# Performance work log

Hardware: AMD Instinct MI355X
Metric: run time of the kernel (lower is better)

## Reference

```python
import jax, jax.numpy as jnp
import numpy as np


def setup_inputs() -> dict:
    key = jax.random.key(0)
    k1, k2 = jax.random.split(key)
    B, C, H = 1024, 1000, 512  # batch, classes, hidden
    y = jax.random.normal(k1, (B, C), dtype=jnp.float32)
    w = jax.random.normal(k2, (C, H), dtype=jnp.float32)
    epsilon = jnp.ones((), dtype=jnp.float32)
    lipschitz = jnp.ones((), dtype=jnp.float32)
    return {"y": y, "w": w, "epsilon": epsilon, "lipschitz": lipschitz}


def reference(y, w, epsilon, lipschitz):
    # y: [B, C] logits; w: [C, H] final-layer weight
    kW = lipschitz * w.T                      # [H, C]
    j = jnp.argmax(y, axis=1)                 # [B]
    y_j = jnp.max(y, axis=1, keepdims=True)   # [B, 1]
    kW_j = kW.T[j]                            # [B, H] gather of argmax column
    kW_ij = kW_j[:, :, None] - kW[None]       # [B, H, C] broadcast difference
    sq = jnp.sum(kW_ij * kW_ij, axis=1)       # [B, C]
    # safe sqrt (value identical; avoids NaN grad at the exact-zero j column)
    K_ij = jnp.where(sq > 0, jnp.sqrt(jnp.where(sq > 0, sq, 1.0)), 0.0)
    y_bot_i = y + epsilon * K_ij              # [B, C]
    y_bot_i = jnp.where(y == y_j, -jnp.inf, y_bot_i)
    y_bot = jnp.max(y_bot_i, axis=1, keepdims=True)  # [B, 1]
    return jnp.concatenate([y, y_bot], axis=1)       # [B, C+1]
```

## Files before the change

### kernel.cpp

```cpp
#include <hip/hip_runtime.h>
#include <math.h>

#define B_SZ 1024
#define C_SZ 1000
#define H_SZ 512


typedef __attribute__((ext_vector_type(8))) short bf16x8;
typedef __attribute__((ext_vector_type(4))) float f32x4;

__global__ __launch_bounds__(256) void k_prep(
    const float* __restrict__ y, const float* __restrict__ w,
    int* __restrict__ jv, float* __restrict__ ymax,
    float* __restrict__ wnorm, short* __restrict__ wbf,
    float* __restrict__ out) {
    const int r = blockIdx.x;
    const int tid = threadIdx.x;
    if (r < 250) {
        const int wave = tid >> 6, lane = tid & 63;
        const int c = r * 4 + wave;
        const float* row = w + c * H_SZ;
        float4 a = *(const float4*)(row + lane * 8);
        float4 b = *(const float4*)(row + lane * 8 + 4);
        float f[8] = {a.x, a.y, a.z, a.w, b.x, b.y, b.z, b.w};
        unsigned short u[8];
        float s = 0.f;
#pragma unroll
        for (int i = 0; i < 8; ++i) {
            s += f[i] * f[i];
            unsigned v = __float_as_uint(f[i]);
            v += 0x7fffu + ((v >> 16) & 1u);
            u[i] = (unsigned short)(v >> 16);
        }
        uint4 pk;
        pk.x = (unsigned)u[0] | ((unsigned)u[1] << 16);
        pk.y = (unsigned)u[2] | ((unsigned)u[3] << 16);
        pk.z = (unsigned)u[4] | ((unsigned)u[5] << 16);
        pk.w = (unsigned)u[6] | ((unsigned)u[7] << 16);
        *(uint4*)(wbf + c * H_SZ + lane * 8) = pk;
#pragma unroll
        for (int off = 32; off; off >>= 1) s += __shfl_down(s, off, 64);
        if (lane == 0) wnorm[c] = s;
    } else {
        const int b = r - 250;
        const float* yrow = y + b * C_SZ;
        float* orow = out + b * (C_SZ + 1);
        float best = -INFINITY;
        int bidx = 0x7fffffff;
        if (tid < 250) {
            float4 v = *(const float4*)(yrow + tid * 4);
            float e[4] = {v.x, v.y, v.z, v.w};
#pragma unroll
            for (int i = 0; i < 4; ++i) {
                orow[tid * 4 + i] = e[i];
                if (e[i] > best) { best = e[i]; bidx = tid * 4 + i; }
            }
        }
        const int lane = tid & 63;
#pragma unroll
        for (int off = 32; off; off >>= 1) {
            float ov = __shfl_down(best, off, 64);
            int oi = __shfl_down(bidx, off, 64);
            if (ov > best || (ov == best && oi < bidx)) { best = ov; bidx = oi; }
        }
        __shared__ float sv[4];
        __shared__ int si[4];
        if (lane == 0) { sv[tid >> 6] = best; si[tid >> 6] = bidx; }
        __syncthreads();
        if (tid == 0) {
            float bv = sv[0]; int bi = si[0];
#pragma unroll
            for (int k = 1; k < 4; ++k) {
                if (sv[k] > bv || (sv[k] == bv && si[k] < bi)) { bv = sv[k]; bi = si[k]; }
            }
            jv[b] = bi;
            ymax[b] = bv;
        }
    }
}

#define KC 128
#define RS 136
__global__ __launch_bounds__(256) void k_main(
    const float* __restrict__ y, const short* __restrict__ wbf,
    const float* __restrict__ eps_p, const float* __restrict__ lip_p,
    const int* __restrict__ jv, const float* __restrict__ ymax,
    const float* __restrict__ wnorm, float* __restrict__ part) {
    __shared__ __align__(16) short Bs[64 * RS];
    __shared__ float snj[64];
    __shared__ float sym[64];

    const int t = threadIdx.x;
    const int bx = blockIdx.x, by = blockIdx.y;
    const int b0 = by * 64, c0 = bx * 64;

    if (t < 64) {
        int j = jv[b0 + t];
        snj[t] = wnorm[j];
        sym[t] = ymax[b0 + t];
    }

    const int wv = t >> 6, lane = t & 63;
    const int col = lane & 15, quad = lane >> 4;

    const int ja = jv[b0 + wv * 16 + col];
    const short* ag = wbf + ja * H_SZ + quad * 8;
    bf16x8 areg[16];
#pragma unroll
    for (int k16 = 0; k16 < 16; ++k16)
        areg[k16] = *(const bf16x8*)(ag + k16 * 32);

    const int srow = t >> 2;
    const int sseg = t & 3;
    int crow = c0 + srow; if (crow > C_SZ - 1) crow = C_SZ - 1;
    const short* bgsrc = wbf + crow * H_SZ;

    uint4 pb[4];
#pragma unroll
    for (int p = 0; p < 4; ++p)
        pb[p] = *(const uint4*)(bgsrc + (sseg + p * 4) * 8);

    const short* brd = &Bs[col * RS + quad * 8];

    f32x4 acc[4] = {{0.f, 0.f, 0.f, 0.f},
                    {0.f, 0.f, 0.f, 0.f},
                    {0.f, 0.f, 0.f, 0.f},
                    {0.f, 0.f, 0.f, 0.f}};

#pragma unroll
    for (int ch = 0; ch < 4; ++ch) {
#pragma unroll
        for (int p = 0; p < 4; ++p)
            *(uint4*)&Bs[srow * RS + (sseg + p * 4) * 8] = pb[p];
        __syncthreads();
        if (ch < 3) {
            const int gbase = (ch + 1) * KC;
#pragma unroll
            for (int p = 0; p < 4; ++p)
                pb[p] = *(const uint4*)(bgsrc + gbase + (sseg + p * 4) * 8);
        }
#pragma unroll
        for (int ks = 0; ks < 4; ++ks) {
            bf16x8 af = areg[ch * 4 + ks];
#pragma unroll
            for (int ct = 0; ct < 4; ++ct) {
                bf16x8 bf = *(const bf16x8*)(brd + ct * 16 * RS + ks * 32);
                acc[ct] =
                    __builtin_amdgcn_mfma_f32_16x16x32_bf16(af, bf, acc[ct], 0, 0, 0);
            }
        }
        __syncthreads();
    }

    const float eps = *eps_p;
    const float L = *lip_p;
    const float L2 = L * L;
    float rmax[4];
#pragma unroll
    for (int i = 0; i < 4; ++i) {
        const int br = wv * 16 + quad * 4 + i;
        const int b = b0 + br;
        const float nj = snj[br];
        const float ym = sym[br];
        float m = -INFINITY;
#pragma unroll
        for (int ct = 0; ct < 4; ++ct) {
            const int cc = c0 + ct * 16 + col;
            if (cc < C_SZ) {
                const float yv = y[b * C_SZ + cc];
                const float nc = wnorm[cc];
                const float sq = L2 * (nj + nc - 2.0f * acc[ct][i]);
                const float K = sq > 0.f ? sqrtf(sq) : 0.f;
                const float cand = (yv == ym) ? -INFINITY : yv + eps * K;
                m = fmaxf(m, cand);
            }
        }
        rmax[i] = m;
    }
#pragma unroll
    for (int off = 8; off; off >>= 1)
#pragma unroll
        for (int i = 0; i < 4; ++i)
            rmax[i] = fmaxf(rmax[i], __shfl_xor(rmax[i], off, 64));
    if (col == 0) {
        float* slice = part + bx * B_SZ;
#pragma unroll
        for (int i = 0; i < 4; ++i)
            slice[b0 + wv * 16 + quad * 4 + i] = rmax[i];
    }
}

__global__ void k_final(const float* __restrict__ part,
                        float* __restrict__ out) {
    int b = blockIdx.x * 256 + threadIdx.x;
    if (b >= B_SZ) return;
    float m = -INFINITY;
#pragma unroll
    for (int s = 0; s < 16; ++s) m = fmaxf(m, part[s * B_SZ + b]);
    out[b * (C_SZ + 1) + C_SZ] = m;
}

extern "C" void kernel_launch(void* const* d_in, const int* in_sizes, int n_in,
                              void* d_out, int out_size, void* d_ws,
                              size_t ws_size, hipStream_t stream) {
    const float* y = (const float*)d_in[0];
    const float* w = (const float*)d_in[1];
    const float* eps = (const float*)d_in[2];
    const float* lip = (const float*)d_in[3];
    float* out = (float*)d_out;

    char* ws = (char*)d_ws;
    int* jv = (int*)ws;
    float* ymax = (float*)(ws + 4096);
    float* wnorm = (float*)(ws + 8192);
    float* part = (float*)(ws + 16384);
    short* wbf = (short*)(ws + 524288);

    k_prep<<<250 + B_SZ, 256, 0, stream>>>(y, w, jv, ymax, wnorm, wbf, out);
    k_main<<<dim3(16, 16), 256, 0, stream>>>(y, wbf, eps, lip, jv, ymax, wnorm,
                                             part);
    k_final<<<(B_SZ + 255) / 256, 256, 0, stream>>>(part, out);
}
```

Before: 79.28 us.

## Fuse prep, main and final kernels into one cooperative kernel with grid syncs

Merges the three kernels into a single cooperative launch of 256 blocks, using grid.sync() between the prep phase (bf16 conversion, norms, per-row argmax), the MFMA distance phase and the final row-max reduction. Row argmax now uses one wave per row instead of one block per row, so 256 blocks cover all 1024 rows. The aim is to remove two kernel launch gaps and the shared-memory cross-wave reduction. In exchange it adds grid-wide barrier costs, and the prep phase now runs on fewer blocks with more serial work per wave.

```diff
diff --git a/kernel.cpp b/kernel.cpp
--- a/kernel.cpp
+++ b/kernel.cpp
@@ -1,5 +1,8 @@
 #include <hip/hip_runtime.h>
+#include <hip/hip_cooperative_groups.h>
 #include <math.h>
+
+namespace cg = cooperative_groups;
 
 #define B_SZ 1024
 #define C_SZ 1000
@@ -9,16 +12,27 @@
 typedef __attribute__((ext_vector_type(8))) short bf16x8;
 typedef __attribute__((ext_vector_type(4))) float f32x4;
 
-__global__ __launch_bounds__(256) void k_prep(
+#define KC 128
+#define RS 136
+
+__global__ __launch_bounds__(256) void k_fused(
     const float* __restrict__ y, const float* __restrict__ w,
+    const float* __restrict__ eps_p, const float* __restrict__ lip_p,
     int* __restrict__ jv, float* __restrict__ ymax,
     float* __restrict__ wnorm, short* __restrict__ wbf,
-    float* __restrict__ out) {
-    const int r = blockIdx.x;
-    const int tid = threadIdx.x;
-    if (r < 250) {
-        const int wave = tid >> 6, lane = tid & 63;
-        const int c = r * 4 + wave;
+    float* __restrict__ part, float* __restrict__ out) {
+    cg::grid_group grid = cg::this_grid();
+
+    __shared__ __align__(16) short Bs[64 * RS];
+    __shared__ float snj[64];
+    __shared__ float sym[64];
+
+    const int blk = blockIdx.x;
+    const int t = threadIdx.x;
+    const int wv = t >> 6, lane = t & 63;
+
+    if (blk < 250) {
+        const int c = blk * 4 + wv;
         const float* row = w + c * H_SZ;
         float4 a = *(const float4*)(row + lane * 8);
         float4 b = *(const float4*)(row + lane * 8 + 4);
@@ -41,57 +55,40 @@
 #pragma unroll
         for (int off = 32; off; off >>= 1) s += __shfl_down(s, off, 64);
         if (lane == 0) wnorm[c] = s;
-    } else {
-        const int b = r - 250;
+    }
+
+    {
+        const int b = blk * 4 + wv;
         const float* yrow = y + b * C_SZ;
         float* orow = out + b * (C_SZ + 1);
         float best = -INFINITY;
         int bidx = 0x7fffffff;
-        if (tid < 250) {
-            float4 v = *(const float4*)(yrow + tid * 4);
-            float e[4] = {v.x, v.y, v.z, v.w};
-#pragma unroll
-            for (int i = 0; i < 4; ++i) {
-                orow[tid * 4 + i] = e[i];
-                if (e[i] > best) { best = e[i]; bidx = tid * 4 + i; }
+#pragma unroll
+        for (int p = 0; p < 4; ++p) {
+            const int idx = lane + p * 64;
+            if (idx < 250) {
+                float4 v = *(const float4*)(yrow + idx * 4);
+                float e[4] = {v.x, v.y, v.z, v.w};
+#pragma unroll
+                for (int i = 0; i < 4; ++i) {
+                    orow[idx * 4 + i] = e[i];
+                    if (e[i] > best) { best = e[i]; bidx = idx * 4 + i; }
+                }
             }
         }
-        const int lane = tid & 63;
 #pragma unroll
         for (int off = 32; off; off >>= 1) {
             float ov = __shfl_down(best, off, 64);
             int oi = __shfl_down(bidx, off, 64);
             if (ov > best || (ov == best && oi < bidx)) { best = ov; bidx = oi; }
         }
-        __shared__ float sv[4];
-        __shared__ int si[4];
-        if (lane == 0) { sv[tid >> 6] = best; si[tid >> 6] = bidx; }
-        __syncthreads();
-        if (tid == 0) {
-            float bv = sv[0]; int bi = si[0];
-#pragma unroll
-            for (int k = 1; k < 4; ++k) {
-                if (sv[k] > bv || (sv[k] == bv && si[k] < bi)) { bv = sv[k]; bi = si[k]; }
-            }
-            jv[b] = bi;
-            ymax[b] = bv;
-        }
-    }
-}
-
-#define KC 128
-#define RS 136
-__global__ __launch_bounds__(256) void k_main(
-    const float* __restrict__ y, const short* __restrict__ wbf,
-    const float* __restrict__ eps_p, const float* __restrict__ lip_p,
-    const int* __restrict__ jv, const float* __restrict__ ymax,
-    const float* __restrict__ wnorm, float* __restrict__ part) {
-    __shared__ __align__(16) short Bs[64 * RS];
-    __shared__ float snj[64];
-    __shared__ float sym[64];
-
-    const int t = threadIdx.x;
-    const int bx = blockIdx.x, by = blockIdx.y;
+        if (lane == 0) { jv[b] = bidx; ymax[b] = best; }
+    }
+
+    __threadfence();
+    grid.sync();
+
+    const int bx = blk & 15, by = blk >> 4;
     const int b0 = by * 64, c0 = bx * 64;
 
     if (t < 64) {
@@ -100,7 +97,6 @@
         sym[t] = ymax[b0 + t];
     }
 
-    const int wv = t >> 6, lane = t & 63;
     const int col = lane & 15, quad = lane >> 4;
 
     const int ja = jv[b0 + wv * 16 + col];
@@ -188,16 +184,19 @@
         for (int i = 0; i < 4; ++i)
             slice[b0 + wv * 16 + quad * 4 + i] = rmax[i];
     }
-}
-
-__global__ void k_final(const float* __restrict__ part,
-                        float* __restrict__ out) {
-    int b = blockIdx.x * 256 + threadIdx.x;
-    if (b >= B_SZ) return;
-    float m = -INFINITY;
-#pragma unroll
-    for (int s = 0; s < 16; ++s) m = fmaxf(m, part[s * B_SZ + b]);
-    out[b * (C_SZ + 1) + C_SZ] = m;
+
+    __threadfence();
+    grid.sync();
+
+    if (t < 64) {
+        const int row = blk * 4 + (t >> 4);
+        const int strip = t & 15;
+        float v = part[strip * B_SZ + row];
+#pragma unroll
+        for (int off = 8; off; off >>= 1)
+            v = fmaxf(v, __shfl_xor(v, off, 64));
+        if (strip == 0) out[row * (C_SZ + 1) + C_SZ] = v;
+    }
 }
 
 extern "C" void kernel_launch(void* const* d_in, const int* in_sizes, int n_in,
@@ -216,8 +215,9 @@
     float* part = (float*)(ws + 16384);
     short* wbf = (short*)(ws + 524288);
 
-    k_prep<<<250 + B_SZ, 256, 0, stream>>>(y, w, jv, ymax, wnorm, wbf, out);
-    k_main<<<dim3(16, 16), 256, 0, stream>>>(y, wbf, eps, lip, jv, ymax, wnorm,
-                                             part);
-    k_final<<<(B_SZ + 255) / 256, 256, 0, stream>>>(part, out);
+    void* args[] = {(void*)&y, (void*)&w, (void*)&eps, (void*)&lip,
+                    (void*)&jv, (void*)&ymax, (void*)&wnorm, (void*)&wbf,
+                    (void*)&part, (void*)&out};
+    hipLaunchCooperativeKernel((const void*)k_fused, dim3(256), dim3(256),
+                               args, 0, stream);
 }
```

Result: slower. 173.3 us (+118.6%).
